# Optimization experiments

Hardware: AMD Instinct MI355X
Metric: run time of the kernel (lower is better)

## Reference

```python
import jax, jax.numpy as jnp
import numpy as np

N_NODES = 100000
N_EDGES = 1600000
IN_F, HID, N_CLS = 512, 64, 32


def gcn_conv(x, edge_index, W, b, num_nodes):
    """PyG GCNConv: h = D^{-1/2} (A+I) D^{-1/2} (x W) + b."""
    loop = jnp.arange(num_nodes)
    src = jnp.concatenate([edge_index[0], loop])  # [E+N]
    dst = jnp.concatenate([edge_index[1], loop])
    # degree of target nodes (incl. self-loops)
    deg = jax.ops.segment_sum(jnp.ones_like(dst, dtype=x.dtype), dst,
                              num_segments=num_nodes)
    dinv = jnp.where(deg > 0, jax.lax.rsqrt(deg), 0.0)
    norm = dinv[src] * dinv[dst]  # [E+N]
    h = x @ W  # dense transform first (matches PyG: small out dim)
    msgs = h[src] * norm[:, None]  # edge-wise gather + scale
    out = jax.ops.segment_sum(msgs, dst, num_segments=num_nodes)  # scatter-add
    return out + b


def setup_inputs() -> dict:
    key = jax.random.key(0)
    k1, k2, k3, k4, k5, k6 = jax.random.split(key, 6)
    x = jax.random.normal(k1, (N_NODES, IN_F), dtype=jnp.float32)
    edge_index = jax.random.randint(k2, (2, N_EDGES), 0, N_NODES, dtype=jnp.int64)
    # Glorot-style init for the two GCNConv weights + biases
    W1 = jax.random.normal(k3, (IN_F, HID), dtype=jnp.float32) / np.sqrt(IN_F)
    b1 = jnp.zeros((HID,), dtype=jnp.float32)
    W2 = jax.random.normal(k4, (HID, N_CLS), dtype=jnp.float32) / np.sqrt(HID)
    b2 = jnp.zeros((N_CLS,), dtype=jnp.float32)
    return {"x": x, "edge_index": edge_index, "W1": W1, "b1": b1,
            "W2": W2, "b2": b2}


def reference(x, edge_index, W1, b1, W2, b2):
    num_nodes = x.shape[0]
    h = jax.nn.relu(gcn_conv(x, edge_index, W1, b1, num_nodes))
    z = gcn_conv(h, edge_index, W2, b2, num_nodes)
    return (h, z)
```

## Files before the change

### kernel.cpp

```cpp
#include <hip/hip_runtime.h>

#define N_NODES 100000
#define N_EDGES 1600000
#define IN_F 512
#define HID 64
#define N_CLS 32
#define NBKT2 391
#define EBLK 8192
#define NBLKA ((N_EDGES + EBLK - 1) / EBLK)

typedef __attribute__((ext_vector_type(8))) short short8;
typedef __attribute__((ext_vector_type(4))) float f32x4;

__device__ __forceinline__ unsigned short f2bf(float f) {
  unsigned int u = __float_as_uint(f);
  u += 0x7FFFu + ((u >> 16) & 1u);
  return (unsigned short)(u >> 16);
}
__device__ __forceinline__ float bf2f(unsigned int s) {
  return __uint_as_float(s << 16);
}

__global__ __launch_bounds__(256) void w1t_k(const float* __restrict__ W1,
                                             unsigned short* __restrict__ W1t,
                                             int* __restrict__ bcnt) {
  int i = blockIdx.x * 256 + threadIdx.x;
  if (i < NBKT2) bcnt[i] = 0;
  if (i < IN_F * HID) {
    int n = i >> 9, k = i & 511;
    W1t[i] = f2bf(W1[(size_t)k * HID + n]);
  }
}

__global__ __launch_bounds__(256) void coarse_hist_k(const int* __restrict__ ei,
                                                     int* __restrict__ bcnt,
                                                     int* __restrict__ bhist) {
  __shared__ int lh[NBKT2];
  int tid = threadIdx.x;
  for (int b = tid; b < NBKT2; b += 256) lh[b] = 0;
  __syncthreads();
  int e0 = blockIdx.x * EBLK;
  int e1 = min(e0 + EBLK, N_EDGES);
  for (int e = e0 + tid; e < e1; e += 256)
    atomicAdd(&lh[ei[N_EDGES + e] >> 8], 1);
  __syncthreads();
  for (int b = tid; b < NBKT2; b += 256) {
    int c = lh[b];
    bhist[blockIdx.x * NBKT2 + b] = c;
    if (c) atomicAdd(&bcnt[b], c);
  }
}

__global__ __launch_bounds__(512) void coarse_scan_k(const int* __restrict__ bcnt,
                                                     int* __restrict__ bbase,
                                                     int* __restrict__ bcur) {
  __shared__ int sc[512];
  int tid = threadIdx.x;
  int v = (tid < NBKT2) ? bcnt[tid] : 0;
  sc[tid] = v;
  __syncthreads();
  for (int off = 1; off < 512; off <<= 1) {
    int t = (tid >= off) ? sc[tid - off] : 0;
    __syncthreads();
    sc[tid] += t;
    __syncthreads();
  }
  int incl = sc[tid];
  int excl = incl - v;
  if (tid < NBKT2) { bbase[tid] = excl; bcur[tid] = excl; }
  if (tid == NBKT2 - 1) bbase[NBKT2] = incl;
}

__global__ __launch_bounds__(256) void passA_k(const int* __restrict__ ei,
                                               const int* __restrict__ bhist,
                                               int* __restrict__ bcur,
                                               unsigned* __restrict__ tmp) {
  __shared__ int gcur[NBKT2];
  int tid = threadIdx.x;
  int e0 = blockIdx.x * EBLK;
  int e1 = min(e0 + EBLK, N_EDGES);
  for (int b = tid; b < NBKT2; b += 256) {
    int c = bhist[blockIdx.x * NBKT2 + b];
    gcur[b] = c ? atomicAdd(&bcur[b], c) : 0;
  }
  __syncthreads();
  for (int e = e0 + tid; e < e1; e += 256) {
    int s = ei[e], d = ei[N_EDGES + e];
    int p = atomicAdd(&gcur[d >> 8], 1);
    tmp[p] = ((unsigned)s << 8) | (unsigned)(d & 255);
  }
}

__global__ __launch_bounds__(256) void passB_k(const unsigned* __restrict__ tmp,
                                               const int* __restrict__ bbase,
                                               int* __restrict__ rowptr,
                                               float* __restrict__ dinv,
                                               int* __restrict__ srcs) {
  __shared__ int sc[256];
  __shared__ int cur[256];
  int b = blockIdx.x, tid = threadIdx.x;
  int n0 = b << 8;
  int n1 = min(n0 + 256, N_NODES);
  int base = bbase[b], end = bbase[b + 1];
  sc[tid] = 0;
  __syncthreads();
  for (int i = base + tid; i < end; i += 256)
    atomicAdd(&sc[tmp[i] & 255u], 1);
  __syncthreads();
  int myc = sc[tid];
  for (int off = 1; off < 256; off <<= 1) {
    int t = (tid >= off) ? sc[tid - off] : 0;
    __syncthreads();
    sc[tid] += t;
    __syncthreads();
  }
  int incl = sc[tid];
  int excl = incl - myc;
  if (n0 + tid < n1) {
    rowptr[n0 + tid + 1] = base + incl;
    dinv[n0 + tid] = rsqrtf((float)(myc + 1));
  }
  if (b == 0 && tid == 0) rowptr[0] = 0;
  cur[tid] = base + excl;
  __syncthreads();
  for (int i = base + tid; i < end; i += 256) {
    unsigned v = tmp[i];
    int p = atomicAdd(&cur[v & 255u], 1);
    srcs[p] = (int)(v >> 8);
  }
}

__global__ __launch_bounds__(256) void gemm1_mfma_k(const float* __restrict__ x,
                                                    const unsigned short* __restrict__ W1t,
                                                    const float* __restrict__ dinv,
                                                    unsigned short* __restrict__ h0s) {
  __shared__ __align__(16) char As[64 * 128];
  __shared__ __align__(16) char Ws[64 * 128];
  int tid = threadIdx.x;
  int wave = tid >> 6, lane = tid & 63;
  int row0 = blockIdx.x * 64;
  f32x4 acc[4] = {{0.f,0.f,0.f,0.f},{0.f,0.f,0.f,0.f},{0.f,0.f,0.f,0.f},{0.f,0.f,0.f,0.f}};

  int l15 = lane & 15, lhi = lane >> 4;
  int rA = (wave << 4) + l15;

  for (int k0 = 0; k0 < IN_F; k0 += 64) {
    #pragma unroll
    for (int i = 0; i < 4; ++i) {
      int f = tid + i * 256;
      int r = f >> 4, c4 = (f & 15) << 2;
      float4 v = make_float4(0.f, 0.f, 0.f, 0.f);
      int gr = row0 + r;
      if (gr < N_NODES) v = *(const float4*)(x + (size_t)gr * IN_F + k0 + c4);
      ushort4 u;
      u.x = f2bf(v.x); u.y = f2bf(v.y); u.z = f2bf(v.z); u.w = f2bf(v.w);
      int byte = r * 128 + (c4 << 1);
      byte ^= (r & 7) << 4;
      *(ushort4*)(As + byte) = u;
    }
    #pragma unroll
    for (int i = 0; i < 2; ++i) {
      int f = tid + i * 256;
      int n = f >> 3, k8 = (f & 7) << 3;
      uint4 v = *(const uint4*)(W1t + (size_t)n * IN_F + k0 + k8);
      int byte = n * 128 + (k8 << 1);
      byte ^= (n & 7) << 4;
      *(uint4*)(Ws + byte) = v;
    }
    __syncthreads();
    #pragma unroll
    for (int ks = 0; ks < 64; ks += 32) {
      int kk = ks + (lhi << 3);
      int ba = rA * 128 + (kk << 1); ba ^= (rA & 7) << 4;
      short8 a = *(const short8*)(As + ba);
      #pragma unroll
      for (int j = 0; j < 4; ++j) {
        int nB = (j << 4) + l15;
        int bb = nB * 128 + (kk << 1); bb ^= (nB & 7) << 4;
        short8 bv = *(const short8*)(Ws + bb);
        acc[j] = __builtin_amdgcn_mfma_f32_16x16x32_bf16(a, bv, acc[j], 0, 0, 0);
      }
    }
    __syncthreads();
  }
  int rbase = row0 + (wave << 4) + (lhi << 2);
  #pragma unroll
  for (int r = 0; r < 4; ++r) {
    int gr = rbase + r;
    if (gr < N_NODES) {
      float dn = dinv[gr];
      #pragma unroll
      for (int j = 0; j < 4; ++j)
        h0s[(size_t)gr * HID + (j << 4) + l15] = f2bf(dn * acc[j][r]);
    }
  }
}

__global__ __launch_bounds__(256) void agg1g2_k(const uint4* __restrict__ h0q,
                                                const int* __restrict__ rowptr,
                                                const int* __restrict__ srcs,
                                                const float* __restrict__ dinv,
                                                const float* __restrict__ b1,
                                                const float* __restrict__ W2,
                                                float* __restrict__ out_h,
                                                unsigned short* __restrict__ h2b) {
  __shared__ float w2s[HID * N_CLS];
  __shared__ float hrow[4][HID];
  int tid = threadIdx.x;
  for (int i = tid; i < HID * N_CLS; i += 256) w2s[i] = W2[i];
  __syncthreads();

  int idx = blockIdx.x * 256 + tid;
  int node = idx >> 6;
  int wv = tid >> 6;
  int lane = tid & 63;
  int fl = lane & 7, g = lane >> 3;
  int p0 = rowptr[node], p1 = rowptr[node + 1];
  int c = p1 - p0;
  int ps = p0 + ((c * g) >> 3);
  int pe = p0 + ((c * (g + 1)) >> 3);
  float a[8] = {0.f,0.f,0.f,0.f,0.f,0.f,0.f,0.f};
  if (g == 0) {
    uint4 u = h0q[(size_t)node * 8 + fl];
    a[0] = bf2f(u.x & 0xffffu); a[1] = bf2f(u.x >> 16);
    a[2] = bf2f(u.y & 0xffffu); a[3] = bf2f(u.y >> 16);
    a[4] = bf2f(u.z & 0xffffu); a[5] = bf2f(u.z >> 16);
    a[6] = bf2f(u.w & 0xffffu); a[7] = bf2f(u.w >> 16);
  }
  int p = ps;
  for (; p + 2 <= pe; p += 2) {
    int s0 = srcs[p], s1 = srcs[p + 1];
    uint4 u0 = h0q[(size_t)s0 * 8 + fl];
    uint4 u1 = h0q[(size_t)s1 * 8 + fl];
    a[0] += bf2f(u0.x & 0xffffu) + bf2f(u1.x & 0xffffu);
    a[1] += bf2f(u0.x >> 16)     + bf2f(u1.x >> 16);
    a[2] += bf2f(u0.y & 0xffffu) + bf2f(u1.y & 0xffffu);
    a[3] += bf2f(u0.y >> 16)     + bf2f(u1.y >> 16);
    a[4] += bf2f(u0.z & 0xffffu) + bf2f(u1.z & 0xffffu);
    a[5] += bf2f(u0.z >> 16)     + bf2f(u1.z >> 16);
    a[6] += bf2f(u0.w & 0xffffu) + bf2f(u1.w & 0xffffu);
    a[7] += bf2f(u0.w >> 16)     + bf2f(u1.w >> 16);
  }
  if (p < pe) {
    uint4 u = h0q[(size_t)srcs[p] * 8 + fl];
    a[0] += bf2f(u.x & 0xffffu); a[1] += bf2f(u.x >> 16);
    a[2] += bf2f(u.y & 0xffffu); a[3] += bf2f(u.y >> 16);
    a[4] += bf2f(u.z & 0xffffu); a[5] += bf2f(u.z >> 16);
    a[6] += bf2f(u.w & 0xffffu); a[7] += bf2f(u.w >> 16);
  }
  #pragma unroll
  for (int off = 8; off < 64; off <<= 1) {
    #pragma unroll
    for (int i = 0; i < 8; ++i) a[i] += __shfl_xor(a[i], off);
  }
  float dn = dinv[node];
  if (g == 0) {
    float4 bA = *(const float4*)(b1 + fl * 8);
    float4 bB = *(const float4*)(b1 + fl * 8 + 4);
    float4 s0, s1;
    s0.x = fmaxf(dn * a[0] + bA.x, 0.f); s0.y = fmaxf(dn * a[1] + bA.y, 0.f);
    s0.z = fmaxf(dn * a[2] + bA.z, 0.f); s0.w = fmaxf(dn * a[3] + bA.w, 0.f);
    s1.x = fmaxf(dn * a[4] + bB.x, 0.f); s1.y = fmaxf(dn * a[5] + bB.y, 0.f);
    s1.z = fmaxf(dn * a[6] + bB.z, 0.f); s1.w = fmaxf(dn * a[7] + bB.w, 0.f);
    *(float4*)(out_h + (size_t)node * HID + fl * 8) = s0;
    *(float4*)(out_h + (size_t)node * HID + fl * 8 + 4) = s1;
    *(float4*)&hrow[wv][fl * 8] = s0;
    *(float4*)&hrow[wv][fl * 8 + 4] = s1;
  }
  int cls = lane & 31, kb = (lane >> 5) << 5;
  float acc2 = 0.f;
  #pragma unroll
  for (int k = 0; k < 32; ++k)
    acc2 += hrow[wv][kb + k] * w2s[(kb + k) * N_CLS + cls];
  acc2 += __shfl_xor(acc2, 32);
  if (lane < 32)
    h2b[(size_t)node * N_CLS + cls] = f2bf(dn * acc2);
}

__global__ __launch_bounds__(256) void agg2_k(const uint2* __restrict__ h2u,
                                              const int* __restrict__ rowptr,
                                              const int* __restrict__ srcs,
                                              const float* __restrict__ dinv,
                                              const float* __restrict__ b2,
                                              float* __restrict__ out) {
  int idx = blockIdx.x * 256 + threadIdx.x;
  int node = idx >> 6;
  if (node >= N_NODES) return;
  int lane = threadIdx.x & 63;
  int fl = lane & 7, g = lane >> 3;
  int p0 = rowptr[node], p1 = rowptr[node + 1];
  int c = p1 - p0;
  int ps = p0 + ((c * g) >> 3);
  int pe = p0 + ((c * (g + 1)) >> 3);
  float a0 = 0.f, a1 = 0.f, a2 = 0.f, a3 = 0.f;
  if (g == 0) {
    uint2 u = h2u[(size_t)node * 8 + fl];
    a0 = bf2f(u.x & 0xffffu); a1 = bf2f(u.x >> 16);
    a2 = bf2f(u.y & 0xffffu); a3 = bf2f(u.y >> 16);
  }
  int p = ps;
  for (; p + 2 <= pe; p += 2) {
    int s0 = srcs[p], s1 = srcs[p + 1];
    uint2 u0 = h2u[(size_t)s0 * 8 + fl];
    uint2 u1 = h2u[(size_t)s1 * 8 + fl];
    a0 += bf2f(u0.x & 0xffffu) + bf2f(u1.x & 0xffffu);
    a1 += bf2f(u0.x >> 16)     + bf2f(u1.x >> 16);
    a2 += bf2f(u0.y & 0xffffu) + bf2f(u1.y & 0xffffu);
    a3 += bf2f(u0.y >> 16)     + bf2f(u1.y >> 16);
  }
  if (p < pe) {
    uint2 u = h2u[(size_t)srcs[p] * 8 + fl];
    a0 += bf2f(u.x & 0xffffu); a1 += bf2f(u.x >> 16);
    a2 += bf2f(u.y & 0xffffu); a3 += bf2f(u.y >> 16);
  }
  #pragma unroll
  for (int off = 8; off < 64; off <<= 1) {
    a0 += __shfl_xor(a0, off); a1 += __shfl_xor(a1, off);
    a2 += __shfl_xor(a2, off); a3 += __shfl_xor(a3, off);
  }
  if (g == 0) {
    float dn = dinv[node];
    float4 bv = *(const float4*)(b2 + fl * 4);
    float4 st;
    st.x = dn * a0 + bv.x; st.y = dn * a1 + bv.y;
    st.z = dn * a2 + bv.z; st.w = dn * a3 + bv.w;
    *(float4*)(out + (size_t)node * N_CLS + fl * 4) = st;
  }
}

extern "C" void kernel_launch(void* const* d_in, const int* in_sizes, int n_in,
                              void* d_out, int out_size, void* d_ws, size_t ws_size,
                              hipStream_t stream) {
  const float* x  = (const float*)d_in[0];
  const int*   ei = (const int*)d_in[1];
  const float* W1 = (const float*)d_in[2];
  const float* b1 = (const float*)d_in[3];
  const float* W2 = (const float*)d_in[4];
  const float* b2 = (const float*)d_in[5];
  float* out_h = (float*)d_out;
  float* out_z = out_h + (size_t)N_NODES * HID;

  char* ws = (char*)d_ws;
  int* bcnt           = (int*)(ws + 0);
  int* bbase          = (int*)(ws + (4 << 10));
  int* bcur           = (int*)(ws + (8 << 10));
  int* bhist          = (int*)(ws + (12 << 10));
  int* rowptr         = (int*)(ws + (336 << 10));
  float* dinv         = (float*)(ws + (752 << 10));
  unsigned short* W1t = (unsigned short*)(ws + (1168 << 10));
  unsigned* tmp       = (unsigned*)(ws + (1280 << 10));
  int* srcs           = (int*)(ws + (8ull << 20));
  unsigned short* h0s = (unsigned short*)(ws + (15ull << 20));
  unsigned short* h2b = (unsigned short*)(ws + (28ull << 20));

  w1t_k<<<(IN_F * HID + 255) / 256, 256, 0, stream>>>(W1, W1t, bcnt);
  coarse_hist_k<<<NBLKA, 256, 0, stream>>>(ei, bcnt, bhist);
  coarse_scan_k<<<1, 512, 0, stream>>>(bcnt, bbase, bcur);
  passA_k<<<NBLKA, 256, 0, stream>>>(ei, bhist, bcur, tmp);
  passB_k<<<NBKT2, 256, 0, stream>>>(tmp, bbase, rowptr, dinv, srcs);
  gemm1_mfma_k<<<(N_NODES + 63) / 64, 256, 0, stream>>>(x, W1t, dinv, h0s);
  agg1g2_k<<<(N_NODES * 64) / 256, 256, 0, stream>>>((const uint4*)h0s, rowptr, srcs,
                                                     dinv, b1, W2, out_h, h2b);
  agg2_k<<<(N_NODES * 64) / 256, 256, 0, stream>>>((const uint2*)h2b, rowptr, srcs,
                                                   dinv, b2, out_z);
}
```

Baseline: 217.2 us.

## Merge CSR build stages with W1 transpose and GEMM1 into fewer launches

Runs the W1 transpose alongside the coarse histogram in one launch. Moves the coarse bucket scan into every passA block, which removes the single-block scan kernel. Runs passA and the dense x·W1 GEMM in the same grid so the edge scatter overlaps the compute-bound GEMM. Because dinv is now unknown when the GEMM runs, the dinv row scaling moves into passB as an extra read-modify-write pass over h0. That costs an extra bf16 rounding and extra memory traffic, and each passA block repeats the small scan redundantly.

```diff
diff --git a/kernel.cpp b/kernel.cpp
--- a/kernel.cpp
+++ b/kernel.cpp
@@ -8,6 +8,8 @@
 #define NBKT2 391
 #define EBLK 8192
 #define NBLKA ((N_EDGES + EBLK - 1) / EBLK)
+#define NBLKW 128
+#define NBLKG ((N_NODES + 63) / 64)
 
 typedef __attribute__((ext_vector_type(8))) short short8;
 typedef __attribute__((ext_vector_type(4))) float f32x4;
@@ -21,73 +23,140 @@
   return __uint_as_float(s << 16);
 }
 
-__global__ __launch_bounds__(256) void w1t_k(const float* __restrict__ W1,
-                                             unsigned short* __restrict__ W1t,
-                                             int* __restrict__ bcnt) {
-  int i = blockIdx.x * 256 + threadIdx.x;
-  if (i < NBKT2) bcnt[i] = 0;
-  if (i < IN_F * HID) {
+__global__ __launch_bounds__(256) void histw1t_k(const int* __restrict__ ei,
+                                                 int* __restrict__ bcnt,
+                                                 int* __restrict__ bhist,
+                                                 const float* __restrict__ W1,
+                                                 unsigned short* __restrict__ W1t) {
+  int tid = threadIdx.x;
+  if (blockIdx.x < NBLKA) {
+    __shared__ int lh[NBKT2];
+    for (int b = tid; b < NBKT2; b += 256) lh[b] = 0;
+    __syncthreads();
+    int e0 = blockIdx.x * EBLK;
+    int e1 = min(e0 + EBLK, N_EDGES);
+    for (int e = e0 + tid; e < e1; e += 256)
+      atomicAdd(&lh[ei[N_EDGES + e] >> 8], 1);
+    __syncthreads();
+    for (int b = tid; b < NBKT2; b += 256) {
+      int c = lh[b];
+      bhist[blockIdx.x * NBKT2 + b] = c;
+      if (c) atomicAdd(&bcnt[b], c);
+    }
+  } else {
+    int i = (blockIdx.x - NBLKA) * 256 + tid;
     int n = i >> 9, k = i & 511;
     W1t[i] = f2bf(W1[(size_t)k * HID + n]);
   }
 }
 
-__global__ __launch_bounds__(256) void coarse_hist_k(const int* __restrict__ ei,
-                                                     int* __restrict__ bcnt,
-                                                     int* __restrict__ bhist) {
-  __shared__ int lh[NBKT2];
+__global__ __launch_bounds__(256) void passAgemm1_k(const int* __restrict__ ei,
+                                                    const int* __restrict__ bcnt,
+                                                    const int* __restrict__ bhist,
+                                                    int* __restrict__ off,
+                                                    int* __restrict__ bbase,
+                                                    unsigned* __restrict__ tmp,
+                                                    const float* __restrict__ x,
+                                                    const unsigned short* __restrict__ W1t,
+                                                    unsigned short* __restrict__ h0s) {
+  __shared__ __align__(16) char smem[64 * 128 * 2];
   int tid = threadIdx.x;
-  for (int b = tid; b < NBKT2; b += 256) lh[b] = 0;
-  __syncthreads();
-  int e0 = blockIdx.x * EBLK;
-  int e1 = min(e0 + EBLK, N_EDGES);
-  for (int e = e0 + tid; e < e1; e += 256)
-    atomicAdd(&lh[ei[N_EDGES + e] >> 8], 1);
-  __syncthreads();
-  for (int b = tid; b < NBKT2; b += 256) {
-    int c = lh[b];
-    bhist[blockIdx.x * NBKT2 + b] = c;
-    if (c) atomicAdd(&bcnt[b], c);
-  }
-}
-
-__global__ __launch_bounds__(512) void coarse_scan_k(const int* __restrict__ bcnt,
-                                                     int* __restrict__ bbase,
-                                                     int* __restrict__ bcur) {
-  __shared__ int sc[512];
-  int tid = threadIdx.x;
-  int v = (tid < NBKT2) ? bcnt[tid] : 0;
-  sc[tid] = v;
-  __syncthreads();
-  for (int off = 1; off < 512; off <<= 1) {
-    int t = (tid >= off) ? sc[tid - off] : 0;
-    __syncthreads();
-    sc[tid] += t;
-    __syncthreads();
-  }
-  int incl = sc[tid];
-  int excl = incl - v;
-  if (tid < NBKT2) { bbase[tid] = excl; bcur[tid] = excl; }
-  if (tid == NBKT2 - 1) bbase[NBKT2] = incl;
-}
-
-__global__ __launch_bounds__(256) void passA_k(const int* __restrict__ ei,
-                                               const int* __restrict__ bhist,
-                                               int* __restrict__ bcur,
-                                               unsigned* __restrict__ tmp) {
-  __shared__ int gcur[NBKT2];
-  int tid = threadIdx.x;
-  int e0 = blockIdx.x * EBLK;
-  int e1 = min(e0 + EBLK, N_EDGES);
-  for (int b = tid; b < NBKT2; b += 256) {
-    int c = bhist[blockIdx.x * NBKT2 + b];
-    gcur[b] = c ? atomicAdd(&bcur[b], c) : 0;
-  }
-  __syncthreads();
-  for (int e = e0 + tid; e < e1; e += 256) {
-    int s = ei[e], d = ei[N_EDGES + e];
-    int p = atomicAdd(&gcur[d >> 8], 1);
-    tmp[p] = ((unsigned)s << 8) | (unsigned)(d & 255);
+
+  if (blockIdx.x < NBLKA) {
+    int* s1   = (int*)smem;
+    int* s2   = s1 + 256;
+    int* bb   = s2 + 256;
+    int* gcur = bb + 400;
+    int a0 = (tid < NBKT2) ? bcnt[tid] : 0;
+    int a1 = (256 + tid < NBKT2) ? bcnt[256 + tid] : 0;
+    s1[tid] = a0; s2[tid] = a1;
+    __syncthreads();
+    for (int o = 1; o < 256; o <<= 1) {
+      int t0 = (tid >= o) ? s1[tid - o] : 0;
+      int t1 = (tid >= o) ? s2[tid - o] : 0;
+      __syncthreads();
+      s1[tid] += t0; s2[tid] += t1;
+      __syncthreads();
+    }
+    int tot0 = s1[255];
+    bb[tid] = s1[tid] - a0;
+    if (256 + tid < NBKT2) bb[256 + tid] = tot0 + s2[tid] - a1;
+    __syncthreads();
+    int rb = blockIdx.x * NBKT2;
+    for (int b = tid; b < NBKT2; b += 256) {
+      int c = bhist[rb + b];
+      gcur[b] = bb[b] + (c ? atomicAdd(&off[b], c) : 0);
+    }
+    if (blockIdx.x == 0) {
+      for (int b = tid; b < NBKT2; b += 256) bbase[b] = bb[b];
+      if (tid == 0) bbase[NBKT2] = N_EDGES;
+    }
+    __syncthreads();
+    int e0 = blockIdx.x * EBLK;
+    int e1 = min(e0 + EBLK, N_EDGES);
+    for (int e = e0 + tid; e < e1; e += 256) {
+      int s = ei[e], d = ei[N_EDGES + e];
+      int p = atomicAdd(&gcur[d >> 8], 1);
+      tmp[p] = ((unsigned)s << 8) | (unsigned)(d & 255);
+    }
+  } else {
+    char* As = smem;
+    char* Ws = smem + 64 * 128;
+    int wave = tid >> 6, lane = tid & 63;
+    int row0 = (blockIdx.x - NBLKA) * 64;
+    f32x4 acc[4] = {{0.f,0.f,0.f,0.f},{0.f,0.f,0.f,0.f},{0.f,0.f,0.f,0.f},{0.f,0.f,0.f,0.f}};
+    int l15 = lane & 15, lhi = lane >> 4;
+    int rA = (wave << 4) + l15;
+
+    for (int k0 = 0; k0 < IN_F; k0 += 64) {
+      #pragma unroll
+      for (int i = 0; i < 4; ++i) {
+        int f = tid + i * 256;
+        int r = f >> 4, c4 = (f & 15) << 2;
+        float4 v = make_float4(0.f, 0.f, 0.f, 0.f);
+        int gr = row0 + r;
+        if (gr < N_NODES) v = *(const float4*)(x + (size_t)gr * IN_F + k0 + c4);
+        ushort4 u;
+        u.x = f2bf(v.x); u.y = f2bf(v.y); u.z = f2bf(v.z); u.w = f2bf(v.w);
+        int byte = r * 128 + (c4 << 1);
+        byte ^= (r & 7) << 4;
+        *(ushort4*)(As + byte) = u;
+      }
+      #pragma unroll
+      for (int i = 0; i < 2; ++i) {
+        int f = tid + i * 256;
+        int n = f >> 3, k8 = (f & 7) << 3;
+        uint4 v = *(const uint4*)(W1t + (size_t)n * IN_F + k0 + k8);
+        int byte = n * 128 + (k8 << 1);
+        byte ^= (n & 7) << 4;
+        *(uint4*)(Ws + byte) = v;
+      }
+      __syncthreads();
+      #pragma unroll
+      for (int ks = 0; ks < 64; ks += 32) {
+        int kk = ks + (lhi << 3);
+        int ba = rA * 128 + (kk << 1); ba ^= (rA & 7) << 4;
+        short8 a = *(const short8*)(As + ba);
+        #pragma unroll
+        for (int j = 0; j < 4; ++j) {
+          int nB = (j << 4) + l15;
+          int bb2 = nB * 128 + (kk << 1); bb2 ^= (nB & 7) << 4;
+          short8 bv = *(const short8*)(Ws + bb2);
+          acc[j] = __builtin_amdgcn_mfma_f32_16x16x32_bf16(a, bv, acc[j], 0, 0, 0);
+        }
+      }
+      __syncthreads();
+    }
+    int rbase = row0 + (wave << 4) + (lhi << 2);
+    #pragma unroll
+    for (int r = 0; r < 4; ++r) {
+      int gr = rbase + r;
+      if (gr < N_NODES) {
+        #pragma unroll
+        for (int j = 0; j < 4; ++j)
+          h0s[(size_t)gr * HID + (j << 4) + l15] = f2bf(acc[j][r]);
+      }
+    }
   }
 }
 
@@ -95,12 +164,15 @@
                                                const int* __restrict__ bbase,
                                                int* __restrict__ rowptr,
                                                float* __restrict__ dinv,
-                                               int* __restrict__ srcs) {
+                                               int* __restrict__ srcs,
+                                               unsigned* __restrict__ h0u) {
   __shared__ int sc[256];
   __shared__ int cur[256];
+  __shared__ float dl[256];
   int b = blockIdx.x, tid = threadIdx.x;
   int n0 = b << 8;
   int n1 = min(n0 + 256, N_NODES);
+  int nn = n1 - n0;
   int base = bbase[b], end = bbase[b + 1];
   sc[tid] = 0;
   __syncthreads();
@@ -108,17 +180,19 @@
     atomicAdd(&sc[tmp[i] & 255u], 1);
   __syncthreads();
   int myc = sc[tid];
-  for (int off = 1; off < 256; off <<= 1) {
-    int t = (tid >= off) ? sc[tid - off] : 0;
+  for (int o = 1; o < 256; o <<= 1) {
+    int t = (tid >= o) ? sc[tid - o] : 0;
     __syncthreads();
     sc[tid] += t;
     __syncthreads();
   }
   int incl = sc[tid];
   int excl = incl - myc;
+  float dn = rsqrtf((float)(myc + 1));
+  dl[tid] = dn;
   if (n0 + tid < n1) {
     rowptr[n0 + tid + 1] = base + incl;
-    dinv[n0 + tid] = rsqrtf((float)(myc + 1));
+    dinv[n0 + tid] = dn;
   }
   if (b == 0 && tid == 0) rowptr[0] = 0;
   cur[tid] = base + excl;
@@ -128,71 +202,14 @@
     int p = atomicAdd(&cur[v & 255u], 1);
     srcs[p] = (int)(v >> 8);
   }
-}
-
-__global__ __launch_bounds__(256) void gemm1_mfma_k(const float* __restrict__ x,
-                                                    const unsigned short* __restrict__ W1t,
-                                                    const float* __restrict__ dinv,
-                                                    unsigned short* __restrict__ h0s) {
-  __shared__ __align__(16) char As[64 * 128];
-  __shared__ __align__(16) char Ws[64 * 128];
-  int tid = threadIdx.x;
-  int wave = tid >> 6, lane = tid & 63;
-  int row0 = blockIdx.x * 64;
-  f32x4 acc[4] = {{0.f,0.f,0.f,0.f},{0.f,0.f,0.f,0.f},{0.f,0.f,0.f,0.f},{0.f,0.f,0.f,0.f}};
-
-  int l15 = lane & 15, lhi = lane >> 4;
-  int rA = (wave << 4) + l15;
-
-  for (int k0 = 0; k0 < IN_F; k0 += 64) {
-    #pragma unroll
-    for (int i = 0; i < 4; ++i) {
-      int f = tid + i * 256;
-      int r = f >> 4, c4 = (f & 15) << 2;
-      float4 v = make_float4(0.f, 0.f, 0.f, 0.f);
-      int gr = row0 + r;
-      if (gr < N_NODES) v = *(const float4*)(x + (size_t)gr * IN_F + k0 + c4);
-      ushort4 u;
-      u.x = f2bf(v.x); u.y = f2bf(v.y); u.z = f2bf(v.z); u.w = f2bf(v.w);
-      int byte = r * 128 + (c4 << 1);
-      byte ^= (r & 7) << 4;
-      *(ushort4*)(As + byte) = u;
-    }
-    #pragma unroll
-    for (int i = 0; i < 2; ++i) {
-      int f = tid + i * 256;
-      int n = f >> 3, k8 = (f & 7) << 3;
-      uint4 v = *(const uint4*)(W1t + (size_t)n * IN_F + k0 + k8);
-      int byte = n * 128 + (k8 << 1);
-      byte ^= (n & 7) << 4;
-      *(uint4*)(Ws + byte) = v;
-    }
-    __syncthreads();
-    #pragma unroll
-    for (int ks = 0; ks < 64; ks += 32) {
-      int kk = ks + (lhi << 3);
-      int ba = rA * 128 + (kk << 1); ba ^= (rA & 7) << 4;
-      short8 a = *(const short8*)(As + ba);
-      #pragma unroll
-      for (int j = 0; j < 4; ++j) {
-        int nB = (j << 4) + l15;
-        int bb = nB * 128 + (kk << 1); bb ^= (nB & 7) << 4;
-        short8 bv = *(const short8*)(Ws + bb);
-        acc[j] = __builtin_amdgcn_mfma_f32_16x16x32_bf16(a, bv, acc[j], 0, 0, 0);
-      }
-    }
-    __syncthreads();
-  }
-  int rbase = row0 + (wave << 4) + (lhi << 2);
-  #pragma unroll
-  for (int r = 0; r < 4; ++r) {
-    int gr = rbase + r;
-    if (gr < N_NODES) {
-      float dn = dinv[gr];
-      #pragma unroll
-      for (int j = 0; j < 4; ++j)
-        h0s[(size_t)gr * HID + (j << 4) + l15] = f2bf(dn * acc[j][r]);
-    }
+  unsigned ub = (unsigned)n0 * 32;
+  int cnt2 = nn * 32;
+  for (int u = tid; u < cnt2; u += 256) {
+    float d = dl[u >> 5];
+    unsigned v = h0u[ub + u];
+    unsigned lo = (unsigned)f2bf(d * bf2f(v & 0xffffu));
+    unsigned hi = (unsigned)f2bf(d * bf2f(v >> 16));
+    h0u[ub + u] = lo | (hi << 16);
   }
 }
 
@@ -342,23 +359,22 @@
 
   char* ws = (char*)d_ws;
   int* bcnt           = (int*)(ws + 0);
-  int* bbase          = (int*)(ws + (4 << 10));
-  int* bcur           = (int*)(ws + (8 << 10));
-  int* bhist          = (int*)(ws + (12 << 10));
-  int* rowptr         = (int*)(ws + (336 << 10));
-  float* dinv         = (float*)(ws + (752 << 10));
-  unsigned short* W1t = (unsigned short*)(ws + (1168 << 10));
+  int* off            = (int*)(ws + 2048);
+  int* bbase          = (int*)(ws + 8192);
+  int* bhist          = (int*)(ws + (16 << 10));
+  int* rowptr         = (int*)(ws + (352 << 10));
+  float* dinv         = (float*)(ws + (768 << 10));
+  unsigned short* W1t = (unsigned short*)(ws + (1184 << 10));
   unsigned* tmp       = (unsigned*)(ws + (1280 << 10));
   int* srcs           = (int*)(ws + (8ull << 20));
   unsigned short* h0s = (unsigned short*)(ws + (15ull << 20));
   unsigned short* h2b = (unsigned short*)(ws + (28ull << 20));
 
-  w1t_k<<<(IN_F * HID + 255) / 256, 256, 0, stream>>>(W1, W1t, bcnt);
-  coarse_hist_k<<<NBLKA, 256, 0, stream>>>(ei, bcnt, bhist);
-  coarse_scan_k<<<1, 512, 0, stream>>>(bcnt, bbase, bcur);
-  passA_k<<<NBLKA, 256, 0, stream>>>(ei, bhist, bcur, tmp);
-  passB_k<<<NBKT2, 256, 0, stream>>>(tmp, bbase, rowptr, dinv, srcs);
-  gemm1_mfma_k<<<(N_NODES + 63) / 64, 256, 0, stream>>>(x, W1t, dinv, h0s);
+  hipMemsetAsync(ws, 0, 4096, stream);
+  histw1t_k<<<NBLKA + NBLKW, 256, 0, stream>>>(ei, bcnt, bhist, W1, W1t);
+  passAgemm1_k<<<NBLKA + NBLKG, 256, 0, stream>>>(ei, bcnt, bhist, off, bbase, tmp,
+                                                  x, W1t, h0s);
+  passB_k<<<NBKT2, 256, 0, stream>>>(tmp, bbase, rowptr, dinv, srcs, (unsigned*)h0s);
   agg1g2_k<<<(N_NODES * 64) / 256, 256, 0, stream>>>((const uint4*)h0s, rowptr, srcs,
                                                      dinv, b1, W2, out_h, h2b);
   agg2_k<<<(N_NODES * 64) / 256, 256, 0, stream>>>((const uint2*)h2b, rowptr, srcs,
```

Result: no change. 215.5 us (-0.8%).
